# Kernel optimization log

Hardware: AMD Instinct MI355X
Metric: run time of the kernel (lower is better)

Reference implementation:

```python
import jax, jax.numpy as jnp
import numpy as np

SIGMA = 0.5
BETA = 0.3
NEG_MODES = 2
EPS = 1e-12


def _l2norm(v, axis):
    n = jnp.sqrt(jnp.sum(v * v, axis=axis, keepdims=True))
    return v / jnp.maximum(n, EPS)


def setup_inputs() -> dict:
    key = jax.random.key(0)
    ks = jax.random.split(key, 6)
    B, Cin, H, W = 16, 256, 64, 64
    E, R = 256, 365
    x = jax.random.normal(ks[0], (B, Cin, H, W), dtype=jnp.float32)
    conv_w = jax.random.normal(ks[1], (E, Cin), dtype=jnp.float32) * 0.02
    conv_b = jax.random.normal(ks[2], (E,), dtype=jnp.float32) * 0.02
    reps = jax.random.normal(ks[3], (R, 1, E), dtype=jnp.float32)
    # stored representations were L2-normalized over the channel dim during training
    representations = _l2norm(reps, axis=2)
    neg_w = jax.random.normal(ks[4], (E * NEG_MODES, E), dtype=jnp.float32) * 0.01
    neg_b = jax.random.normal(ks[5], (E * NEG_MODES,), dtype=jnp.float32) * 0.01
    return {"x": x, "conv_w": conv_w, "conv_b": conv_b,
            "representations": representations, "neg_w": neg_w, "neg_b": neg_b}


def _distance(reps, emb):
    # reps: [R, M, E], emb: [B, E, H, W] (both unit-normalized)
    # ||e - r||^2 = ||e||^2 + ||r||^2 - 2 e.r  -- avoids the 6D broadcast tensor
    dot = jnp.einsum('behw,rme->brmhw', emb, reps)
    en2 = jnp.sum(emb * emb, axis=1)          # [B, H, W]
    rn2 = jnp.sum(reps * reps, axis=2)        # [R, M]
    d2 = en2[:, None, None] + rn2[None, :, :, None, None] - 2.0 * dot
    return jnp.sqrt(jnp.maximum(d2, 0.0))


def reference(x, conv_w, conv_b, representations, neg_w, neg_b):
    # emb_module: 1x1 conv, then L2-normalize over channels (dim=1)
    emb = jnp.einsum('bchw,ec->behw', x, conv_w) + conv_b[None, :, None, None]
    emb = _l2norm(emb, axis=1)

    reps = jax.lax.stop_gradient(representations)        # [R, 1, E] (detached)
    R, _, E = reps.shape
    neg_offset = (jnp.abs(reps[:, 0, :]) @ neg_w.T + neg_b).reshape(R, NEG_MODES, E)
    reps_neg = (neg_offset + jnp.abs(reps)) * jnp.sign(reps)   # broadcast [R,1,E]->[R,2,E]
    reps_neg = _l2norm(reps_neg, axis=2)

    distance = _distance(reps, emb)          # [B, R, 1, H, W]
    distance_neg = _distance(reps_neg, emb)  # [B, R, 2, H, W]

    inv2s2 = 1.0 / (2.0 * SIGMA ** 2)
    probs_neg = jnp.exp(-(distance_neg ** 2) * inv2s2)
    cls_score_neg = jnp.max(probs_neg, axis=2)               # [B, R, H, W]
    probs_ori = jnp.max(jnp.exp(-(distance ** 2) * inv2s2), axis=2)

    dn_min = jnp.min(distance_neg, axis=2, keepdims=True)    # [B, R, 1, H, W]
    probs = jnp.exp(-((distance + BETA * (2.0 - dn_min)) ** 2) * inv2s2)

    # cls_norm=True branch
    probs_sumj = jnp.sum(probs, axis=2)                      # [B, R, H, W]
    probs_sumij = jnp.sum(probs_sumj, axis=1, keepdims=True)
    cls_score = probs_sumj / probs_sumij

    return (cls_score, cls_score_neg, distance, distance_neg, probs_ori)
```

## Files before the change

### kernel.cpp

```cpp
#include <hip/hip_runtime.h>

#define BATCH   16
#define CIN     256
#define EDIM    256
#define HW      4096
#define NPIX    65536
#define RREAL   365
#define RPAD    368
#define NCHUNK  23
#define OUTPLANE 23920640

typedef __attribute__((ext_vector_type(8))) short short8;
typedef __attribute__((ext_vector_type(4))) float f32x4;

__device__ __forceinline__ unsigned short f2bf(float f) {
    union { float f; unsigned u; } v; v.f = f;
    unsigned r = v.u + 0x7fffu + ((v.u >> 16) & 1u);
    return (unsigned short)(r >> 16);
}

__global__ void k_cvt_w(const float* __restrict__ w, unsigned short* __restrict__ wbf) {
    int i = blockIdx.x * 256 + threadIdx.x;
    wbf[i] = f2bf(w[i]);
}

__global__ __launch_bounds__(256) void k_reps(const float* __restrict__ reps,
                                              const float* __restrict__ negw,
                                              const float* __restrict__ negb,
                                              unsigned short* __restrict__ rp,
                                              unsigned short* __restrict__ rn0,
                                              unsigned short* __restrict__ rn1) {
    int r = blockIdx.x;
    int t = threadIdx.x;
    if (r >= RREAL) {
        rp[r*256 + t] = 0; rn0[r*256 + t] = 0; rn1[r*256 + t] = 0;
        return;
    }
    __shared__ __align__(16) float sa[256];
    __shared__ float red[8];
    float rv = reps[r*256 + t];
    float av = fabsf(rv);
    sa[t] = av;
    __syncthreads();
    const float4* a4 = (const float4*)sa;
    const float4* w0 = (const float4*)(negw + (size_t)t * 256);
    const float4* w1 = (const float4*)(negw + (size_t)(256 + t) * 256);
    float acc0 = negb[t], acc1 = negb[256 + t];
    #pragma unroll 8
    for (int k = 0; k < 64; k++) {
        float4 a = a4[k];
        float4 x0 = w0[k], x1 = w1[k];
        acc0 += a.x*x0.x + a.y*x0.y + a.z*x0.z + a.w*x0.w;
        acc1 += a.x*x1.x + a.y*x1.y + a.z*x1.z + a.w*x1.w;
    }
    float sgn = (rv > 0.f) ? 1.f : ((rv < 0.f) ? -1.f : 0.f);
    float v0 = (acc0 + av) * sgn;
    float v1 = (acc1 + av) * sgn;
    float s0 = v0*v0, s1 = v1*v1;
    #pragma unroll
    for (int off = 32; off; off >>= 1) { s0 += __shfl_xor(s0, off); s1 += __shfl_xor(s1, off); }
    int wid = t >> 6;
    if ((t & 63) == 0) { red[wid] = s0; red[4 + wid] = s1; }
    __syncthreads();
    float t0 = red[0] + red[1] + red[2] + red[3];
    float t1 = red[4] + red[5] + red[6] + red[7];
    float i0 = 1.f / fmaxf(sqrtf(t0), 1e-12f);
    float i1 = 1.f / fmaxf(sqrtf(t1), 1e-12f);
    rp [r*256 + t] = f2bf(rv);
    rn0[r*256 + t] = f2bf(v0 * i0);
    rn1[r*256 + t] = f2bf(v1 * i1);
}

__global__ __launch_bounds__(256) void k_conv(const float* __restrict__ x,
                                              const unsigned short* __restrict__ wbf,
                                              const float* __restrict__ convb,
                                              unsigned short* __restrict__ emb) {
    int wave = threadIdx.x >> 6, lane = threadIdx.x & 63;
    int l15 = lane & 15, quad = lane >> 4;
    int px0 = blockIdx.x * 64 + wave * 16;
    int b = px0 >> 12, hw0 = px0 & 4095;
    const float* xb = x + (size_t)b * CIN * HW;
    int hwa = hw0 + l15;

    f32x4 acc[16];
    #pragma unroll
    for (int et = 0; et < 16; et++) acc[et] = (f32x4){0.f, 0.f, 0.f, 0.f};

    for (int k0 = 0; k0 < 8; k0++) {
        int c0 = k0 * 32 + quad * 8;
        short8 af;
        #pragma unroll
        for (int j = 0; j < 8; j++) {
            float xv = xb[(size_t)(c0 + j) * HW + hwa];
            ((unsigned short*)&af)[j] = f2bf(xv);
        }
        #pragma unroll
        for (int et = 0; et < 16; et++) {
            short8 bf = *(const short8*)(wbf + (size_t)(et*16 + l15) * 256 + k0*32 + quad*8);
            acc[et] = __builtin_amdgcn_mfma_f32_16x16x32_bf16(af, bf, acc[et], 0, 0, 0);
        }
    }
    #pragma unroll
    for (int reg = 0; reg < 4; reg++) {
        int px = px0 + quad * 4 + reg;
        float v[16];
        float s = 0.f;
        #pragma unroll
        for (int et = 0; et < 16; et++) {
            float vv = acc[et][reg] + convb[et*16 + l15];
            v[et] = vv; s += vv * vv;
        }
        s += __shfl_xor(s, 1); s += __shfl_xor(s, 2);
        s += __shfl_xor(s, 4); s += __shfl_xor(s, 8);
        float inv = 1.f / fmaxf(sqrtf(s), 1e-12f);
        #pragma unroll
        for (int et = 0; et < 16; et++)
            emb[(size_t)px * 256 + et*16 + l15] = f2bf(v[et] * inv);
    }
}

__global__ __launch_bounds__(256) void k_main(const unsigned short* __restrict__ emb,
                                              const unsigned short* __restrict__ rp,
                                              const unsigned short* __restrict__ rn0,
                                              const unsigned short* __restrict__ rn1,
                                              float* __restrict__ oCls,
                                              float* __restrict__ oClsNeg,
                                              float* __restrict__ oDist,
                                              float* __restrict__ oDneg,
                                              float* __restrict__ oPori,
                                              float* __restrict__ sumij) {
    int wave = threadIdx.x >> 6, lane = threadIdx.x & 63;
    int l15 = lane & 15, quad = lane >> 4;
    int px0 = blockIdx.x * 64 + wave * 16;
    int b = px0 >> 12, hw0 = px0 & 4095;
    int hw = hw0 + l15;
    size_t obase = (size_t)b * RREAL * HW;

    short8 ef[8];
    #pragma unroll
    for (int k0 = 0; k0 < 8; k0++)
        ef[k0] = *(const short8*)(emb + (size_t)(px0 + l15) * 256 + k0*32 + quad*8);

    float sumP = 0.f;
    for (int ch = 0; ch < NCHUNK; ch++) {
        int r0 = ch * 16;
        f32x4 aP  = (f32x4){0.f,0.f,0.f,0.f};
        f32x4 aN0 = (f32x4){0.f,0.f,0.f,0.f};
        f32x4 aN1 = (f32x4){0.f,0.f,0.f,0.f};
        size_t rrow = (size_t)(r0 + l15) * 256 + quad * 8;
        #pragma unroll
        for (int k0 = 0; k0 < 8; k0++) {
            short8 fp = *(const short8*)(rp  + rrow + k0*32);
            short8 f0 = *(const short8*)(rn0 + rrow + k0*32);
            short8 f1 = *(const short8*)(rn1 + rrow + k0*32);
            aP  = __builtin_amdgcn_mfma_f32_16x16x32_bf16(fp, ef[k0], aP , 0, 0, 0);
            aN0 = __builtin_amdgcn_mfma_f32_16x16x32_bf16(f0, ef[k0], aN0, 0, 0, 0);
            aN1 = __builtin_amdgcn_mfma_f32_16x16x32_bf16(f1, ef[k0], aN1, 0, 0, 0);
        }
        #pragma unroll
        for (int reg = 0; reg < 4; reg++) {
            int r = r0 + quad * 4 + reg;
            float d2 = fmaxf(2.f - 2.f * aP[reg], 0.f);
            float e0 = fmaxf(2.f - 2.f * aN0[reg], 0.f);
            float e1 = fmaxf(2.f - 2.f * aN1[reg], 0.f);
            float d   = sqrtf(d2);
            float dn0 = sqrtf(e0);
            float dn1 = sqrtf(e1);
            float pori = __expf(-2.f * d2);
            float pn0  = __expf(-2.f * e0);
            float pn1  = __expf(-2.f * e1);
            float clsneg = fmaxf(pn0, pn1);
            float dnmin  = fminf(dn0, dn1);
            float tt = fmaf(-0.3f, dnmin, d + 0.6f);
            float probs = __expf(-2.f * tt * tt);
            if (r < RREAL) {
                size_t idx = obase + ((size_t)r << 12) + hw;
                oDist[idx]   = d;
                oPori[idx]   = pori;
                oClsNeg[idx] = clsneg;
                oCls[idx]    = probs;
                size_t idn = obase * 2 + ((size_t)(r * 2) << 12) + hw;
                oDneg[idn]        = dn0;
                oDneg[idn + HW]   = dn1;
                sumP += probs;
            }
        }
    }
    sumP += __shfl_xor(sumP, 16);
    sumP += __shfl_xor(sumP, 32);
    if (lane < 16) sumij[px0 + lane] = sumP;
}

__global__ void k_div(float* __restrict__ oCls, const float* __restrict__ sumij) {
    size_t base = ((size_t)blockIdx.x * 256 + threadIdx.x) * 4;
    float4 p = *(float4*)(oCls + base);
    int b  = (int)(base / ((size_t)RREAL * HW));
    int hw = (int)(base & 4095);
    float4 s = *(const float4*)(sumij + b * HW + hw);
    p.x /= s.x; p.y /= s.y; p.z /= s.z; p.w /= s.w;
    *(float4*)(oCls + base) = p;
}

extern "C" void kernel_launch(void* const* d_in, const int* in_sizes, int n_in,
                              void* d_out, int out_size, void* d_ws, size_t ws_size,
                              hipStream_t stream) {
    const float* x      = (const float*)d_in[0];
    const float* conv_w = (const float*)d_in[1];
    const float* conv_b = (const float*)d_in[2];
    const float* reps   = (const float*)d_in[3];
    const float* neg_w  = (const float*)d_in[4];
    const float* neg_b  = (const float*)d_in[5];
    float* out = (float*)d_out;

    char* ws = (char*)d_ws;
    unsigned short* emb = (unsigned short*)ws;
    unsigned short* rp  = (unsigned short*)(ws + 33554432);
    unsigned short* rn0 = rp  + RPAD * 256;
    unsigned short* rn1 = rn0 + RPAD * 256;
    unsigned short* wbf = rn1 + RPAD * 256;
    float* sumij = (float*)(ws + 33554432 + 3 * RPAD * 256 * 2 + 65536 * 2);

    float* oCls    = out;
    float* oClsNeg = out + (size_t)OUTPLANE;
    float* oDist   = out + (size_t)OUTPLANE * 2;
    float* oDneg   = out + (size_t)OUTPLANE * 3;
    float* oPori   = out + (size_t)OUTPLANE * 5;

    k_cvt_w<<<256, 256, 0, stream>>>(conv_w, wbf);
    k_reps <<<RPAD, 256, 0, stream>>>(reps, neg_w, neg_b, rp, rn0, rn1);
    k_conv <<<NPIX / 64, 256, 0, stream>>>(x, wbf, conv_b, emb);
    k_main <<<NPIX / 64, 256, 0, stream>>>(emb, rp, rn0, rn1,
                                           oCls, oClsNeg, oDist, oDneg, oPori, sumij);
    k_div  <<<OUTPLANE / 1024, 256, 0, stream>>>(oCls, sumij);
}
```

Baseline: 940.9 us.

## Fuse conv and distance kernels, transpose MFMA for vectorized output stores

Merges the 1x1 conv + L2 norm kernel with the distance kernel, so the normalized embedding goes through LDS instead of a global round trip. It also swaps the MFMA operand order so each lane holds 4 consecutive pixels and can write float4 stores to the large output planes. The weight conversion is folded into the reps kernel, whose GEMV now uses coalesced row reads with wave reductions. The divide kernel gets a 2D grid. Together these cut launch count, the intermediate embedding traffic and scalar store overhead, at the cost of more LDS use and register pressure in the fused kernel.

```diff
diff --git a/kernel.cpp b/kernel.cpp
--- a/kernel.cpp
+++ b/kernel.cpp
@@ -9,6 +9,7 @@
 #define RPAD    368
 #define NCHUNK  23
 #define OUTPLANE 23920640
+#define ESTRIDE 264
 
 typedef __attribute__((ext_vector_type(8))) short short8;
 typedef __attribute__((ext_vector_type(4))) float f32x4;
@@ -19,47 +20,47 @@
     return (unsigned short)(r >> 16);
 }
 
-__global__ void k_cvt_w(const float* __restrict__ w, unsigned short* __restrict__ wbf) {
-    int i = blockIdx.x * 256 + threadIdx.x;
-    wbf[i] = f2bf(w[i]);
-}
-
 __global__ __launch_bounds__(256) void k_reps(const float* __restrict__ reps,
                                               const float* __restrict__ negw,
                                               const float* __restrict__ negb,
+                                              const float* __restrict__ convw,
+                                              unsigned short* __restrict__ wbf,
                                               unsigned short* __restrict__ rp,
                                               unsigned short* __restrict__ rn0,
                                               unsigned short* __restrict__ rn1) {
     int r = blockIdx.x;
     int t = threadIdx.x;
+    if (r < 256) wbf[r*256 + t] = f2bf(convw[r*256 + t]);
     if (r >= RREAL) {
         rp[r*256 + t] = 0; rn0[r*256 + t] = 0; rn1[r*256 + t] = 0;
         return;
     }
     __shared__ __align__(16) float sa[256];
+    __shared__ float outo[512];
     __shared__ float red[8];
     float rv = reps[r*256 + t];
     float av = fabsf(rv);
     sa[t] = av;
     __syncthreads();
-    const float4* a4 = (const float4*)sa;
-    const float4* w0 = (const float4*)(negw + (size_t)t * 256);
-    const float4* w1 = (const float4*)(negw + (size_t)(256 + t) * 256);
-    float acc0 = negb[t], acc1 = negb[256 + t];
-    #pragma unroll 8
-    for (int k = 0; k < 64; k++) {
-        float4 a = a4[k];
-        float4 x0 = w0[k], x1 = w1[k];
-        acc0 += a.x*x0.x + a.y*x0.y + a.z*x0.z + a.w*x0.w;
-        acc1 += a.x*x1.x + a.y*x1.y + a.z*x1.z + a.w*x1.w;
-    }
+    int wid = t >> 6, lane = t & 63;
+    const f32x4* a4 = (const f32x4*)sa;
+    f32x4 a = a4[lane];
+    #pragma unroll 4
+    for (int i = 0; i < 128; i++) {
+        int e = wid*128 + i;
+        f32x4 wv = *(const f32x4*)(negw + (size_t)e*256 + lane*4);
+        float p = wv[0]*a[0] + wv[1]*a[1] + wv[2]*a[2] + wv[3]*a[3];
+        #pragma unroll
+        for (int off = 32; off; off >>= 1) p += __shfl_xor(p, off);
+        if (lane == 0) outo[e] = p + negb[e];
+    }
+    __syncthreads();
     float sgn = (rv > 0.f) ? 1.f : ((rv < 0.f) ? -1.f : 0.f);
-    float v0 = (acc0 + av) * sgn;
-    float v1 = (acc1 + av) * sgn;
+    float v0 = (outo[t] + av) * sgn;
+    float v1 = (outo[256 + t] + av) * sgn;
     float s0 = v0*v0, s1 = v1*v1;
     #pragma unroll
     for (int off = 32; off; off >>= 1) { s0 += __shfl_xor(s0, off); s1 += __shfl_xor(s1, off); }
-    int wid = t >> 6;
     if ((t & 63) == 0) { red[wid] = s0; red[4 + wid] = s1; }
     __syncthreads();
     float t0 = red[0] + red[1] + red[2] + red[3];
@@ -71,10 +72,19 @@
     rn1[r*256 + t] = f2bf(v1 * i1);
 }
 
-__global__ __launch_bounds__(256) void k_conv(const float* __restrict__ x,
-                                              const unsigned short* __restrict__ wbf,
-                                              const float* __restrict__ convb,
-                                              unsigned short* __restrict__ emb) {
+__global__ __launch_bounds__(256) void k_fused(const float* __restrict__ x,
+                                               const unsigned short* __restrict__ wbf,
+                                               const float* __restrict__ convb,
+                                               const unsigned short* __restrict__ rp,
+                                               const unsigned short* __restrict__ rn0,
+                                               const unsigned short* __restrict__ rn1,
+                                               float* __restrict__ oCls,
+                                               float* __restrict__ oClsNeg,
+                                               float* __restrict__ oDist,
+                                               float* __restrict__ oDneg,
+                                               float* __restrict__ oPori,
+                                               float* __restrict__ sumij) {
+    __shared__ unsigned short elds[4][16][ESTRIDE];
     int wave = threadIdx.x >> 6, lane = threadIdx.x & 63;
     int l15 = lane & 15, quad = lane >> 4;
     int px0 = blockIdx.x * 64 + wave * 16;
@@ -85,7 +95,6 @@
     f32x4 acc[16];
     #pragma unroll
     for (int et = 0; et < 16; et++) acc[et] = (f32x4){0.f, 0.f, 0.f, 0.f};
-
     for (int k0 = 0; k0 < 8; k0++) {
         int c0 = k0 * 32 + quad * 8;
         short8 af;
@@ -100,14 +109,16 @@
             acc[et] = __builtin_amdgcn_mfma_f32_16x16x32_bf16(af, bf, acc[et], 0, 0, 0);
         }
     }
+    float cb[16];
+    #pragma unroll
+    for (int et = 0; et < 16; et++) cb[et] = convb[et*16 + l15];
     #pragma unroll
     for (int reg = 0; reg < 4; reg++) {
-        int px = px0 + quad * 4 + reg;
-        float v[16];
-        float s = 0.f;
+        int pl = quad * 4 + reg;
+        float v[16]; float s = 0.f;
         #pragma unroll
         for (int et = 0; et < 16; et++) {
-            float vv = acc[et][reg] + convb[et*16 + l15];
+            float vv = acc[et][reg] + cb[et];
             v[et] = vv; s += vv * vv;
         }
         s += __shfl_xor(s, 1); s += __shfl_xor(s, 2);
@@ -115,90 +126,89 @@
         float inv = 1.f / fmaxf(sqrtf(s), 1e-12f);
         #pragma unroll
         for (int et = 0; et < 16; et++)
-            emb[(size_t)px * 256 + et*16 + l15] = f2bf(v[et] * inv);
-    }
-}
-
-__global__ __launch_bounds__(256) void k_main(const unsigned short* __restrict__ emb,
-                                              const unsigned short* __restrict__ rp,
-                                              const unsigned short* __restrict__ rn0,
-                                              const unsigned short* __restrict__ rn1,
-                                              float* __restrict__ oCls,
-                                              float* __restrict__ oClsNeg,
-                                              float* __restrict__ oDist,
-                                              float* __restrict__ oDneg,
-                                              float* __restrict__ oPori,
-                                              float* __restrict__ sumij) {
-    int wave = threadIdx.x >> 6, lane = threadIdx.x & 63;
-    int l15 = lane & 15, quad = lane >> 4;
-    int px0 = blockIdx.x * 64 + wave * 16;
-    int b = px0 >> 12, hw0 = px0 & 4095;
-    int hw = hw0 + l15;
+            elds[wave][pl][et*16 + l15] = f2bf(v[et] * inv);
+    }
+    __syncthreads();
+
+    short8 ef[8];
+    #pragma unroll
+    for (int k0 = 0; k0 < 8; k0++)
+        ef[k0] = *(const short8*)&elds[wave][l15][k0*32 + quad*8];
+
     size_t obase = (size_t)b * RREAL * HW;
-
-    short8 ef[8];
-    #pragma unroll
-    for (int k0 = 0; k0 < 8; k0++)
-        ef[k0] = *(const short8*)(emb + (size_t)(px0 + l15) * 256 + k0*32 + quad*8);
-
-    float sumP = 0.f;
+    int hwq = hw0 + quad * 4;
+    size_t rowb = obase        + ((size_t)l15 << 12) + hwq;
+    size_t idnb = (obase << 1) + ((size_t)l15 << 13) + hwq;
+    f32x4 sumP = (f32x4){0.f, 0.f, 0.f, 0.f};
+
     for (int ch = 0; ch < NCHUNK; ch++) {
-        int r0 = ch * 16;
+        int r = ch * 16 + l15;
+        size_t rrow = (size_t)r * 256 + quad * 8;
         f32x4 aP  = (f32x4){0.f,0.f,0.f,0.f};
         f32x4 aN0 = (f32x4){0.f,0.f,0.f,0.f};
         f32x4 aN1 = (f32x4){0.f,0.f,0.f,0.f};
-        size_t rrow = (size_t)(r0 + l15) * 256 + quad * 8;
         #pragma unroll
         for (int k0 = 0; k0 < 8; k0++) {
             short8 fp = *(const short8*)(rp  + rrow + k0*32);
             short8 f0 = *(const short8*)(rn0 + rrow + k0*32);
             short8 f1 = *(const short8*)(rn1 + rrow + k0*32);
-            aP  = __builtin_amdgcn_mfma_f32_16x16x32_bf16(fp, ef[k0], aP , 0, 0, 0);
-            aN0 = __builtin_amdgcn_mfma_f32_16x16x32_bf16(f0, ef[k0], aN0, 0, 0, 0);
-            aN1 = __builtin_amdgcn_mfma_f32_16x16x32_bf16(f1, ef[k0], aN1, 0, 0, 0);
-        }
-        #pragma unroll
-        for (int reg = 0; reg < 4; reg++) {
-            int r = r0 + quad * 4 + reg;
-            float d2 = fmaxf(2.f - 2.f * aP[reg], 0.f);
-            float e0 = fmaxf(2.f - 2.f * aN0[reg], 0.f);
-            float e1 = fmaxf(2.f - 2.f * aN1[reg], 0.f);
+            aP  = __builtin_amdgcn_mfma_f32_16x16x32_bf16(ef[k0], fp, aP , 0, 0, 0);
+            aN0 = __builtin_amdgcn_mfma_f32_16x16x32_bf16(ef[k0], f0, aN0, 0, 0, 0);
+            aN1 = __builtin_amdgcn_mfma_f32_16x16x32_bf16(ef[k0], f1, aN1, 0, 0, 0);
+        }
+        f32x4 vD, vPori, vCneg, vCls, vDn0, vDn1;
+        #pragma unroll
+        for (int c = 0; c < 4; c++) {
+            float d2 = fmaxf(2.f - 2.f * aP [c], 0.f);
+            float e0 = fmaxf(2.f - 2.f * aN0[c], 0.f);
+            float e1 = fmaxf(2.f - 2.f * aN1[c], 0.f);
             float d   = sqrtf(d2);
             float dn0 = sqrtf(e0);
             float dn1 = sqrtf(e1);
-            float pori = __expf(-2.f * d2);
-            float pn0  = __expf(-2.f * e0);
-            float pn1  = __expf(-2.f * e1);
-            float clsneg = fmaxf(pn0, pn1);
-            float dnmin  = fminf(dn0, dn1);
+            vD[c]    = d;
+            vDn0[c]  = dn0;
+            vDn1[c]  = dn1;
+            vPori[c] = __expf(-2.f * d2);
+            float pn0 = __expf(-2.f * e0);
+            float pn1 = __expf(-2.f * e1);
+            vCneg[c] = fmaxf(pn0, pn1);
+            float dnmin = fminf(dn0, dn1);
             float tt = fmaf(-0.3f, dnmin, d + 0.6f);
-            float probs = __expf(-2.f * tt * tt);
-            if (r < RREAL) {
-                size_t idx = obase + ((size_t)r << 12) + hw;
-                oDist[idx]   = d;
-                oPori[idx]   = pori;
-                oClsNeg[idx] = clsneg;
-                oCls[idx]    = probs;
-                size_t idn = obase * 2 + ((size_t)(r * 2) << 12) + hw;
-                oDneg[idn]        = dn0;
-                oDneg[idn + HW]   = dn1;
-                sumP += probs;
-            }
-        }
-    }
-    sumP += __shfl_xor(sumP, 16);
-    sumP += __shfl_xor(sumP, 32);
-    if (lane < 16) sumij[px0 + lane] = sumP;
-}
-
-__global__ void k_div(float* __restrict__ oCls, const float* __restrict__ sumij) {
-    size_t base = ((size_t)blockIdx.x * 256 + threadIdx.x) * 4;
-    float4 p = *(float4*)(oCls + base);
-    int b  = (int)(base / ((size_t)RREAL * HW));
-    int hw = (int)(base & 4095);
-    float4 s = *(const float4*)(sumij + b * HW + hw);
-    p.x /= s.x; p.y /= s.y; p.z /= s.z; p.w /= s.w;
-    *(float4*)(oCls + base) = p;
+            vCls[c]  = __expf(-2.f * tt * tt);
+        }
+        if (r < RREAL) {
+            size_t row = rowb + ((size_t)ch << 16);
+            *(f32x4*)(oDist   + row) = vD;
+            *(f32x4*)(oPori   + row) = vPori;
+            *(f32x4*)(oClsNeg + row) = vCneg;
+            *(f32x4*)(oCls    + row) = vCls;
+            size_t idn = idnb + ((size_t)ch << 17);
+            *(f32x4*)(oDneg + idn)      = vDn0;
+            *(f32x4*)(oDneg + idn + HW) = vDn1;
+            sumP += vCls;
+        }
+    }
+    #pragma unroll
+    for (int off = 1; off <= 8; off <<= 1) {
+        sumP[0] += __shfl_xor(sumP[0], off);
+        sumP[1] += __shfl_xor(sumP[1], off);
+        sumP[2] += __shfl_xor(sumP[2], off);
+        sumP[3] += __shfl_xor(sumP[3], off);
+    }
+    if (l15 == 0)
+        *(f32x4*)(sumij + px0 + quad * 4) = sumP;
+}
+
+__global__ __launch_bounds__(256) void k_div(float* __restrict__ oCls,
+                                             const float* __restrict__ sumij) {
+    int bb = blockIdx.y;
+    size_t off = (size_t)blockIdx.x * 1024 + threadIdx.x * 4;
+    int hw = (int)(off & 4095);
+    float* p = oCls + (size_t)bb * ((size_t)RREAL * HW) + off;
+    f32x4 v = *(f32x4*)p;
+    f32x4 s = *(const f32x4*)(sumij + bb * HW + hw);
+    v[0] /= s[0]; v[1] /= s[1]; v[2] /= s[2]; v[3] /= s[3];
+    *(f32x4*)p = v;
 }
 
 extern "C" void kernel_launch(void* const* d_in, const int* in_sizes, int n_in,
@@ -213,12 +223,11 @@
     float* out = (float*)d_out;
 
     char* ws = (char*)d_ws;
-    unsigned short* emb = (unsigned short*)ws;
-    unsigned short* rp  = (unsigned short*)(ws + 33554432);
+    unsigned short* rp  = (unsigned short*)ws;
     unsigned short* rn0 = rp  + RPAD * 256;
     unsigned short* rn1 = rn0 + RPAD * 256;
     unsigned short* wbf = rn1 + RPAD * 256;
-    float* sumij = (float*)(ws + 33554432 + 3 * RPAD * 256 * 2 + 65536 * 2);
+    float* sumij = (float*)(ws + 3 * RPAD * 256 * 2 + 65536 * 2);
 
     float* oCls    = out;
     float* oClsNeg = out + (size_t)OUTPLANE;
@@ -226,10 +235,8 @@
     float* oDneg   = out + (size_t)OUTPLANE * 3;
     float* oPori   = out + (size_t)OUTPLANE * 5;
 
-    k_cvt_w<<<256, 256, 0, stream>>>(conv_w, wbf);
-    k_reps <<<RPAD, 256, 0, stream>>>(reps, neg_w, neg_b, rp, rn0, rn1);
-    k_conv <<<NPIX / 64, 256, 0, stream>>>(x, wbf, conv_b, emb);
-    k_main <<<NPIX / 64, 256, 0, stream>>>(emb, rp, rn0, rn1,
+    k_reps <<<RPAD, 256, 0, stream>>>(reps, neg_w, neg_b, conv_w, wbf, rp, rn0, rn1);
+    k_fused<<<NPIX / 64, 256, 0, stream>>>(x, wbf, conv_b, rp, rn0, rn1,
                                            oCls, oClsNeg, oDist, oDneg, oPori, sumij);
-    k_div  <<<OUTPLANE / 1024, 256, 0, stream>>>(oCls, sumij);
-}
+    k_div  <<<dim3(RREAL * HW / 1024, BATCH), 256, 0, stream>>>(oCls, sumij);
+}
```

New measurement: 953.6 us. Within noise of the previous version (+1.3%).
